# Optimization experiments

Hardware: AMD Instinct MI355X
Metric: run time of the kernel (lower is better)

The kernel has to match this reference:

```python
import jax, jax.numpy as jnp
import numpy as np

B, L, D, DI = 2, 2048, 1024, 2048  # batch, seq, d_model, d_inner = d_model*expand
EPS = 1e-5
N_ITERS = 30  # fixed-point iterations (no_grad phase); original iterates to convergence (max_iter cap)


def _shift(h):
    # shift(h, 1, dim=1): h_t <- h_{t-1}, zero at t=0
    return jnp.concatenate([jnp.zeros_like(h[:, :1]), h[:, :-1]], axis=1)


def _linrec(inputs, coeffs):
    # h_t = coeffs_t * h_{t-1} + inputs_t along seq axis (axis=1)
    def comb(l, r):
        a1, b1 = l
        a2, b2 = r
        return a2 * a1, a2 * b1 + b2
    _, h = jax.lax.associative_scan(comb, (coeffs, inputs), axis=1)
    return h


def _fp_step(x_i, b, lam, W_v, b_v, h_prev):
    # channel mixing: rank-1 selective Householder reflection of delta_x,
    # parameterized by concat([x_mixer, shift(h_prev)]) (mixer_h_dep, not symm)
    h_sh = _shift(h_prev)
    param = jnp.concatenate([x_i, h_sh], axis=-1)            # [B,L,2*DI]
    v = jax.nn.silu(param @ W_v + b_v)                        # [B,L,DI]
    v = v / (jnp.linalg.norm(v, axis=-1, keepdims=True) + EPS)
    dx = b * x_i - h_prev
    mixed = dx - 2.0 * jnp.sum(dx * v, axis=-1, keepdims=True) * v
    x_tilde = mixed + h_prev
    # sequence mixing: h_t = lam_t * h_{t-1} + (1-lam_t) * x_tilde_t
    return _linrec((1.0 - lam) * x_tilde, lam)


def setup_inputs() -> dict:
    key = jax.random.key(0)
    ks = jax.random.split(key, 8)
    def w(k, shape, fan_in):
        return (jax.random.normal(k, shape, jnp.float32) / np.sqrt(fan_in)).astype(jnp.float32)
    return {
        "x": jax.random.normal(ks[0], (B, L, D), jnp.float32),
        "W_in": w(ks[1], (D, 2 * DI), D),          # input_trans (no bias)
        "W_b": w(ks[2], (DI, DI), DI),              # b_proj (no bias)
        "W_lam": w(ks[3], (DI, DI), DI),            # lambda_proj
        "b_lam": jnp.zeros((DI,), jnp.float32),
        "W_v": w(ks[4], (2 * DI, DI), 2 * DI),      # mixer householder vector proj
        "b_v": jnp.zeros((DI,), jnp.float32),
        "W_c": w(ks[5], (2 * DI, DI), 2 * DI),      # c_proj (no bias)
        "g_norm": jnp.ones((DI,), jnp.float32),     # RMSNorm weight
        "W_out": w(ks[6], (DI, D), DI),             # output_trans (no bias)
    }


def reference(x, W_in, W_b, W_lam, b_lam, W_v, b_v, W_c, g_norm, W_out):
    xz = x @ W_in                                   # [B,L,2*DI]
    x_i, z = xz[..., :DI], xz[..., DI:]
    # no short conv: x_mixer = x_b = x_lambda = x_i
    b = jax.nn.silu(x_i @ W_b)
    lam = jax.nn.sigmoid(x_i @ W_lam + b_lam)

    step = lambda h: _fp_step(x_i, b, lam, W_v, b_v, h)
    # fixed-point iteration (no grad in original)
    h0 = jax.lax.fori_loop(0, N_ITERS, lambda i, h: step(h), jnp.zeros_like(x_i))
    # n_backwards = 1 differentiable step
    h = step(h0)

    x_c = jnp.concatenate([x_i, _shift(h)], axis=-1)
    c = jax.nn.silu(x_c @ W_c)
    y = c * h
    u = jax.nn.silu(z) * y
    u = u * jax.lax.rsqrt(jnp.mean(u * u, axis=-1, keepdims=True) + EPS) * g_norm  # RMSNorm
    return u @ W_out
```

## Files before the change

kernel.cpp:

```cpp
#include <hip/hip_runtime.h>
#include <hip/hip_bf16.h>
#include <hip/hip_fp16.h>

#define DI     2048
#define LSEQ   2048
#define NBATCH 2
#define MROWS  4096
#define EPSF   1e-5f
#define NSTEPS 31
#define NCH    64
#define CL     32

typedef float    f32x4 __attribute__((ext_vector_type(4)));
typedef float    f32x2 __attribute__((ext_vector_type(2)));
typedef _Float16 f16x8 __attribute__((ext_vector_type(8)));
typedef _Float16 f16x2 __attribute__((ext_vector_type(2)));
using f16 = _Float16;

constexpr size_t MB = 1024ull * 1024ull;
constexpr size_t OFF_APARAM = 0;
constexpr size_t OFF_WVT    = OFF_APARAM + 32 * MB;
constexpr size_t OFF_WCT    = OFF_WVT    + 16 * MB;
constexpr size_t OFF_WBT    = OFF_WCT    + 16 * MB;
constexpr size_t OFF_WLT    = OFF_WBT    +  8 * MB;
constexpr size_t OFF_WINT   = OFF_WLT    +  8 * MB;
constexpr size_t OFF_WOT    = OFF_WINT   +  8 * MB;
constexpr size_t OFF_AX     = OFF_WOT    +  4 * MB;
constexpr size_t OFF_Z      = OFF_AX     +  8 * MB;
constexpr size_t OFF_U      = OFF_Z      + 16 * MB;
constexpr size_t OFF_XI     = OFF_U      + 16 * MB;
constexpr size_t OFF_BX     = OFF_XI     + 32 * MB;
constexpr size_t OFF_LAM    = OFF_BX     + 32 * MB;
constexpr size_t OFF_H      = OFF_LAM    + 32 * MB;
constexpr size_t OFF_VRAW   = OFF_H      + 32 * MB;
constexpr size_t OFF_VX     = OFF_VRAW   + 32 * MB;
constexpr size_t OFF_INP    = OFF_VX     + 32 * MB;
constexpr size_t OFF_SSP    = OFF_INP    + 32 * MB;
constexpr size_t OFF_DRP    = OFF_SSP    + (size_t)4096*32*4;
constexpr size_t OFF_CA     = OFF_DRP    + (size_t)4096*32*4;
constexpr size_t OFF_CB     = OFF_CA     + (size_t)NBATCH*NCH*2048*4;
constexpr size_t OFF_CAR    = OFF_CB     + (size_t)NBATCH*NCH*2048*4;
constexpr size_t ARENA_SZ   = OFF_CAR    + (size_t)NBATCH*NCH*2048*4;

__device__ __align__(256) char g_buf[ARENA_SZ];

__device__ __forceinline__ void gload16(const void* g, void* l) {
  __builtin_amdgcn_global_load_lds((const __attribute__((address_space(1))) void*)g,
                                   (__attribute__((address_space(3))) void*)l, 16, 0, 0);
}
__device__ __forceinline__ float siluf(float x) { return x / (1.0f + __expf(-x)); }
__device__ __forceinline__ float sigmf(float x) { return 1.0f / (1.0f + __expf(-x)); }

template<int EPI>
__global__ __launch_bounds__(256) void gemm_f16(
    const f16* __restrict__ A, int lda,
    const f16* __restrict__ Bt, int ldb,
    int N, int K,
    float* __restrict__ outf,
    f16* __restrict__ outb,
    f16* __restrict__ outb2,
    const float* __restrict__ aux0,
    const float* __restrict__ aux1,
    const float* __restrict__ aux2,
    const f16* __restrict__ auxb,
    float* __restrict__ ssp,
    float* __restrict__ drp)
{
  __shared__ char As[2][128 * 64 * 2];
  __shared__ char Bs[2][128 * 64 * 2];

  const int tid = threadIdx.x;
  const int l   = tid & 63;
  const int w   = tid >> 6;
  const int wm  = (w >> 1) << 6;
  const int wn  = (w & 1) << 6;
  const int ntn = N >> 7;
  const int nwg = (int)gridDim.x;
  const int id  = (blockIdx.x & 7) * (nwg >> 3) + (blockIdx.x >> 3);
  const int bm  = id / ntn;
  const int bn  = id % ntn;
  const size_t m0 = (size_t)bm << 7;
  const size_t n0 = (size_t)bn << 7;

  const char* Ab = (const char*)A + m0 * (size_t)(lda * 2);
  const char* Bb = (const char*)Bt + n0 * (size_t)(ldb * 2);

  f32x4 acc[4][4];
#pragma unroll
  for (int i = 0; i < 4; ++i)
#pragma unroll
    for (int j = 0; j < 4; ++j) acc[i][j] = (f32x4){0.f, 0.f, 0.f, 0.f};

  auto stage = [&](int bf, int kte) {
#pragma unroll
    for (int rep = 0; rep < 4; ++rep) {
      const int o   = tid + (rep << 8);
      const int r   = o >> 3;
      const int cb  = (o & 7) << 4;
      const int scb = cb ^ ((r & 7) << 4);
      gload16(Ab + (size_t)r * (size_t)(lda * 2) + (size_t)kte * 2 + scb, &As[bf][o << 4]);
      gload16(Bb + (size_t)r * (size_t)(ldb * 2) + (size_t)kte * 2 + scb, &Bs[bf][o << 4]);
    }
  };

  const int nt = K >> 6;
  stage(0, 0);
  for (int t = 0; t < nt; ++t) {
    const int cur = t & 1;
    if (t + 1 < nt) {
      stage(cur ^ 1, (t + 1) << 6);
      asm volatile("s_waitcnt vmcnt(8)" ::: "memory");
    } else {
      asm volatile("s_waitcnt vmcnt(0)" ::: "memory");
    }
    __builtin_amdgcn_s_barrier();
    __builtin_amdgcn_sched_barrier(0);
    const char* Asc = As[cur];
    const char* Bsc = Bs[cur];
#pragma unroll
    for (int kk = 0; kk < 2; ++kk) {
      f16x8 af[4], bfr[4];
      const int kb = (kk << 6) + ((l >> 4) << 4);
#pragma unroll
      for (int i = 0; i < 4; ++i) {
        const int Ra = wm + (i << 4) + (l & 15);
        af[i]  = *(const f16x8*)(Asc + (Ra << 7) + (kb ^ ((Ra & 7) << 4)));
        const int Rb = wn + (i << 4) + (l & 15);
        bfr[i] = *(const f16x8*)(Bsc + (Rb << 7) + (kb ^ ((Rb & 7) << 4)));
      }
#pragma unroll
      for (int i = 0; i < 4; ++i)
#pragma unroll
        for (int j = 0; j < 4; ++j)
          acc[i][j] = __builtin_amdgcn_mfma_f32_16x16x32_f16(af[i], bfr[j], acc[i][j], 0, 0, 0);
    }
    __builtin_amdgcn_sched_barrier(0);
    __builtin_amdgcn_s_barrier();
    __builtin_amdgcn_sched_barrier(0);
  }

  if constexpr (EPI == 4) {
#pragma unroll
    for (int i = 0; i < 4; ++i) {
#pragma unroll
      for (int rg = 0; rg < 4; ++rg) {
        const size_t row = m0 + wm + (i << 4) + ((l >> 4) << 2) + rg;
        float ssl = 0.f, drl = 0.f;
#pragma unroll
        for (int j = 0; j < 4; ++j) {
          const size_t col = n0 + wn + (j << 4) + (l & 15);
          const size_t idx = (row << 11) + col;
          const float v = siluf(acc[i][j][rg] + aux2[idx]);
          outf[idx] = v;
          ssl += v * v;
          drl += (aux0[idx] - aux1[idx]) * v;
        }
#pragma unroll
        for (int m = 8; m; m >>= 1) {
          ssl += __shfl_xor(ssl, m);
          drl += __shfl_xor(drl, m);
        }
        if ((l & 15) == 0) {
          const int nb2 = (bn << 1) + (wn >> 6);
          ssp[(row << 5) + nb2] = ssl;
          drp[(row << 5) + nb2] = drl;
        }
      }
    }
  } else {
#pragma unroll
    for (int i = 0; i < 4; ++i) {
#pragma unroll
      for (int j = 0; j < 4; ++j) {
#pragma unroll
        for (int rg = 0; rg < 4; ++rg) {
          const size_t row = m0 + wm + (i << 4) + ((l >> 4) << 2) + rg;
          const size_t col = n0 + wn + (j << 4) + (l & 15);
          const float v = acc[i][j][rg];
          if constexpr (EPI == 0) {
            outf[row * (size_t)N + col] = v;
          } else if constexpr (EPI == 1) {
            if (col < DI) {
              outf[(row << 11) + col] = v;
              outb[(row << 12) + col] = (f16)v;
            } else {
              outb2[(row << 11) + (col - DI)] = (f16)v;
            }
          } else if constexpr (EPI == 2) {
            const size_t idx = (row << 11) + col;
            outf[idx] = siluf(v) * aux0[idx];
          } else if constexpr (EPI == 3) {
            outf[(row << 11) + col] = sigmf(v + aux1[col]);
          } else if constexpr (EPI == 5) {
            const size_t idx = (row << 11) + col;
            outf[idx] = siluf(v) * aux0[idx] * siluf((float)auxb[idx]);
          } else if constexpr (EPI == 6) {
            const size_t idx = (row << 11) + col;
            outf[idx] = v + aux1[col];
          }
        }
      }
    }
  }
}

__global__ __launch_bounds__(256) void transpose_f32_f16(
    const float* __restrict__ in, f16* __restrict__ out, int R, int C)
{
  __shared__ float t[32][33];
  const int bx = blockIdx.x * 32;
  const int by = blockIdx.y * 32;
  const int lx = threadIdx.x;
  const int ly = threadIdx.y;
#pragma unroll
  for (int i = 0; i < 32; i += 8)
    t[ly + i][lx] = in[(size_t)(by + ly + i) * C + bx + lx];
  __syncthreads();
#pragma unroll
  for (int i = 0; i < 32; i += 8)
    out[(size_t)(bx + ly + i) * R + by + lx] = (f16)t[lx][ly + i];
}

__global__ __launch_bounds__(256) void cast_f32_f16(
    const float* __restrict__ in, f16* __restrict__ out, int n)
{
  const int i = blockIdx.x * 256 + threadIdx.x;
  if (i < n) out[i] = (f16)in[i];
}

__global__ __launch_bounds__(256) void fill_init(
    float* __restrict__ h, f16* __restrict__ Aparam)
{
  const int idx = blockIdx.x * 256 + threadIdx.x;
  h[idx] = 0.0f;
  const int r = idx >> 11, c = idx & 2047;
  Aparam[((size_t)r << 12) + DI + c] = (f16)0.0f;
}

__global__ __launch_bounds__(256) void scan_k1(
    const float* __restrict__ vraw, const float* __restrict__ bx,
    const float* __restrict__ lam,
    const float* __restrict__ ssp, const float* __restrict__ drp,
    float* __restrict__ inp, float* __restrict__ cA, float* __restrict__ cB)
{
  const int bid = blockIdx.x;
  const int g  = bid & 3;
  const int ch = (bid >> 2) & (NCH - 1);
  const int b  = bid >> 8;
  const int tid = threadIdx.x;
  const int d = (g << 9) + (tid << 1);

  __shared__ float sc_s[CL];
  if (tid < CL) {
    const int grow = b * LSEQ + ch * CL + tid;
    float ss = 0.f, dr = 0.f;
#pragma unroll
    for (int p = 0; p < 32; ++p) {
      ss += ssp[(grow << 5) + p];
      dr += drp[(grow << 5) + p];
    }
    const float n = sqrtf(ss) + EPSF;
    sc_s[tid] = 2.0f * dr / (n * n);
  }
  __syncthreads();

  const size_t base = ((size_t)(b * LSEQ + ch * CL) << 11) + d;
  float hv0 = 0.f, hv1 = 0.f, A0 = 1.f, A1 = 1.f;
#pragma unroll 4
  for (int t = 0; t < CL; ++t) {
    const size_t ix = base + ((size_t)t << 11);
    const f32x2 la = *(const f32x2*)&lam[ix];
    const f32x2 v  = *(const f32x2*)&vraw[ix];
    const f32x2 bb = *(const f32x2*)&bx[ix];
    const float sc = sc_s[t];
    const float i0 = (1.0f - la.x) * (bb.x - sc * v.x);
    const float i1 = (1.0f - la.y) * (bb.y - sc * v.y);
    *(f32x2*)&inp[ix] = (f32x2){i0, i1};
    hv0 = la.x * hv0 + i0;
    hv1 = la.y * hv1 + i1;
    A0 *= la.x;
    A1 *= la.y;
  }
  const size_t ci = ((size_t)(b * NCH + ch) << 11) + d;
  *(f32x2*)&cA[ci] = (f32x2){A0, A1};
  *(f32x2*)&cB[ci] = (f32x2){hv0, hv1};
}

__global__ __launch_bounds__(256) void scan_carry(
    const float* __restrict__ cA, const float* __restrict__ cB,
    float* __restrict__ carry)
{
  const int idx = blockIdx.x * 256 + threadIdx.x;
  const int b = idx >> 11, d = idx & 2047;
  float cur = 0.f;
  for (int ch = 0; ch < NCH; ++ch) {
    const size_t ci = ((size_t)(b * NCH + ch) << 11) + d;
    carry[ci] = cur;
    cur = cA[ci] * cur + cB[ci];
  }
}

__global__ __launch_bounds__(256) void scan_k2(
    const float* __restrict__ inp, const float* __restrict__ lam,
    const float* __restrict__ carry,
    float* __restrict__ h, f16* __restrict__ Aparam)
{
  const int bid = blockIdx.x;
  const int g  = bid & 3;
  const int ch = (bid >> 2) & (NCH - 1);
  const int b  = bid >> 8;
  const int tid = threadIdx.x;
  const int d = (g << 9) + (tid << 1);

  const size_t ci = ((size_t)(b * NCH + ch) << 11) + d;
  const f32x2 cr = *(const f32x2*)&carry[ci];
  float hv0 = cr.x, hv1 = cr.y;

  const size_t base = ((size_t)(b * LSEQ + ch * CL) << 11) + d;
#pragma unroll 4
  for (int t = 0; t < CL; ++t) {
    const size_t ix = base + ((size_t)t << 11);
    const f32x2 la = *(const f32x2*)&lam[ix];
    const f32x2 ii = *(const f32x2*)&inp[ix];
    hv0 = la.x * hv0 + ii.x;
    hv1 = la.y * hv1 + ii.y;
    *(f32x2*)&h[ix] = (f32x2){hv0, hv1};
    const int tg = ch * CL + t;
    if (tg < LSEQ - 1)
      *(f16x2*)&Aparam[(((size_t)(b * LSEQ + tg + 1)) << 12) + DI + d] =
          (f16x2){(f16)hv0, (f16)hv1};
  }
}

__global__ __launch_bounds__(256) void rms_norm(
    const float* __restrict__ uraw, const float* __restrict__ gn,
    f16* __restrict__ u)
{
  const int row = blockIdx.x;
  const size_t base = (size_t)row << 11;
  const int tid = threadIdx.x;
  float uv[8];
  float ss = 0.f;
#pragma unroll
  for (int k = 0; k < 8; ++k) {
    const int c = tid + (k << 8);
    uv[k] = uraw[base + c];
    ss += uv[k] * uv[k];
  }
#pragma unroll
  for (int off = 32; off; off >>= 1) ss += __shfl_xor(ss, off);
  __shared__ float sred[4];
  const int l = tid & 63, w = tid >> 6;
  if (l == 0) sred[w] = ss;
  __syncthreads();
  ss = sred[0] + sred[1] + sred[2] + sred[3];
  const float scale = 1.0f / sqrtf(ss * (1.0f / DI) + EPSF);
#pragma unroll
  for (int k = 0; k < 8; ++k) {
    const int c = tid + (k << 8);
    u[base + c] = (f16)(uv[k] * scale * gn[c]);
  }
}

extern "C" void kernel_launch(void* const* d_in, const int* in_sizes, int n_in,
                              void* d_out, int out_size, void* d_ws, size_t ws_size,
                              hipStream_t stream)
{
  (void)in_sizes; (void)n_in; (void)out_size; (void)d_ws; (void)ws_size;
  const float* x      = (const float*)d_in[0];
  const float* W_in   = (const float*)d_in[1];
  const float* W_b    = (const float*)d_in[2];
  const float* W_lam  = (const float*)d_in[3];
  const float* b_lam  = (const float*)d_in[4];
  const float* W_v    = (const float*)d_in[5];
  const float* b_v    = (const float*)d_in[6];
  const float* W_c    = (const float*)d_in[7];
  const float* g_norm = (const float*)d_in[8];
  const float* W_out  = (const float*)d_in[9];
  float* out = (float*)d_out;

  char* buf = nullptr;
  hipGetSymbolAddress((void**)&buf, HIP_SYMBOL(g_buf));

  f16* Aparam = (f16*)(buf + OFF_APARAM);
  f16* Wvt    = (f16*)(buf + OFF_WVT);
  f16* Wct    = (f16*)(buf + OFF_WCT);
  f16* Wbt    = (f16*)(buf + OFF_WBT);
  f16* Wlt    = (f16*)(buf + OFF_WLT);
  f16* Wint   = (f16*)(buf + OFF_WINT);
  f16* Wot    = (f16*)(buf + OFF_WOT);
  f16* Ax     = (f16*)(buf + OFF_AX);
  f16* Zb     = (f16*)(buf + OFF_Z);
  f16* Ub     = (f16*)(buf + OFF_U);
  float* xi   = (float*)(buf + OFF_XI);
  float* bx   = (float*)(buf + OFF_BX);
  float* lam  = (float*)(buf + OFF_LAM);
  float* h    = (float*)(buf + OFF_H);
  float* vraw = (float*)(buf + OFF_VRAW);
  float* vx   = (float*)(buf + OFF_VX);
  float* inp  = (float*)(buf + OFF_INP);
  float* ssp  = (float*)(buf + OFF_SSP);
  float* drp  = (float*)(buf + OFF_DRP);
  float* cA   = (float*)(buf + OFF_CA);
  float* cB   = (float*)(buf + OFF_CB);
  float* car  = (float*)(buf + OFF_CAR);

  const dim3 b256(256);
  const dim3 tb(32, 8);

  fill_init<<<dim3(MROWS * DI / 256), b256, 0, stream>>>(h, Aparam);

  transpose_f32_f16<<<dim3(4096 / 32, 1024 / 32), tb, 0, stream>>>(W_in,  Wint, 1024, 4096);
  transpose_f32_f16<<<dim3(2048 / 32, 2048 / 32), tb, 0, stream>>>(W_b,   Wbt,  2048, 2048);
  transpose_f32_f16<<<dim3(2048 / 32, 2048 / 32), tb, 0, stream>>>(W_lam, Wlt,  2048, 2048);
  transpose_f32_f16<<<dim3(2048 / 32, 4096 / 32), tb, 0, stream>>>(W_v,   Wvt,  4096, 2048);
  transpose_f32_f16<<<dim3(2048 / 32, 4096 / 32), tb, 0, stream>>>(W_c,   Wct,  4096, 2048);
  transpose_f32_f16<<<dim3(1024 / 32, 2048 / 32), tb, 0, stream>>>(W_out, Wot,  2048, 1024);
  cast_f32_f16<<<dim3(MROWS * 1024 / 256), b256, 0, stream>>>(x, Ax, MROWS * 1024);

  gemm_f16<1><<<dim3(32 * 32), b256, 0, stream>>>(Ax, 1024, Wint, 1024, 4096, 1024,
      xi, Aparam, Zb, nullptr, nullptr, nullptr, nullptr, nullptr, nullptr);
  gemm_f16<2><<<dim3(32 * 16), b256, 0, stream>>>(Aparam, 4096, Wbt, 2048, 2048, 2048,
      bx, nullptr, nullptr, xi, nullptr, nullptr, nullptr, nullptr, nullptr);
  gemm_f16<3><<<dim3(32 * 16), b256, 0, stream>>>(Aparam, 4096, Wlt, 2048, 2048, 2048,
      lam, nullptr, nullptr, nullptr, b_lam, nullptr, nullptr, nullptr, nullptr);
  gemm_f16<6><<<dim3(32 * 16), b256, 0, stream>>>(Aparam, 4096, Wvt, 4096, 2048, 2048,
      vx, nullptr, nullptr, nullptr, b_v, nullptr, nullptr, nullptr, nullptr);

  for (int s = 0; s < NSTEPS; ++s) {
    gemm_f16<4><<<dim3(32 * 16), b256, 0, stream>>>(Aparam + DI, 4096, Wvt + DI, 4096, 2048, 2048,
        vraw, nullptr, nullptr, bx, h, vx, nullptr, ssp, drp);
    scan_k1<<<dim3(NBATCH * NCH * 4), b256, 0, stream>>>(vraw, bx, lam, ssp, drp, inp, cA, cB);
    scan_carry<<<dim3(16), b256, 0, stream>>>(cA, cB, car);
    scan_k2<<<dim3(NBATCH * NCH * 4), b256, 0, stream>>>(inp, lam, car, h, Aparam);
  }

  gemm_f16<5><<<dim3(32 * 16), b256, 0, stream>>>(Aparam, 4096, Wct, 4096, 2048, 4096,
      vraw, nullptr, nullptr, h, nullptr, nullptr, Zb, nullptr, nullptr);
  rms_norm<<<dim3(MROWS), b256, 0, stream>>>(vraw, g_norm, Ub);
  gemm_f16<0><<<dim3(32 * 8), b256, 0, stream>>>(Ub, 2048, Wot, 2048, 1024, 2048,
      out, nullptr, nullptr, nullptr, nullptr, nullptr, nullptr, nullptr, nullptr);
}
```

Before: 3.701 ms.

## Use 8-wave GEMM blocks and fold carry scan into second scan pass

```diff
diff --git a/kernel.cpp b/kernel.cpp
--- a/kernel.cpp
+++ b/kernel.cpp
@@ -36,11 +36,10 @@
 constexpr size_t OFF_VX     = OFF_VRAW   + 32 * MB;
 constexpr size_t OFF_INP    = OFF_VX     + 32 * MB;
 constexpr size_t OFF_SSP    = OFF_INP    + 32 * MB;
-constexpr size_t OFF_DRP    = OFF_SSP    + (size_t)4096*32*4;
-constexpr size_t OFF_CA     = OFF_DRP    + (size_t)4096*32*4;
+constexpr size_t OFF_DRP    = OFF_SSP    + (size_t)4096*64*4;
+constexpr size_t OFF_CA     = OFF_DRP    + (size_t)4096*64*4;
 constexpr size_t OFF_CB     = OFF_CA     + (size_t)NBATCH*NCH*2048*4;
-constexpr size_t OFF_CAR    = OFF_CB     + (size_t)NBATCH*NCH*2048*4;
-constexpr size_t ARENA_SZ   = OFF_CAR    + (size_t)NBATCH*NCH*2048*4;
+constexpr size_t ARENA_SZ   = OFF_CB     + (size_t)NBATCH*NCH*2048*4;
 
 __device__ __align__(256) char g_buf[ARENA_SZ];
 
@@ -52,7 +51,7 @@
 __device__ __forceinline__ float sigmf(float x) { return 1.0f / (1.0f + __expf(-x)); }
 
 template<int EPI>
-__global__ __launch_bounds__(256) void gemm_f16(
+__global__ __launch_bounds__(512) void gemm_f16(
     const f16* __restrict__ A, int lda,
     const f16* __restrict__ Bt, int ldb,
     int N, int K,
@@ -72,8 +71,8 @@
   const int tid = threadIdx.x;
   const int l   = tid & 63;
   const int w   = tid >> 6;
-  const int wm  = (w >> 1) << 6;
-  const int wn  = (w & 1) << 6;
+  const int wm  = (w >> 2) << 6;
+  const int wn  = (w & 3) << 5;
   const int ntn = N >> 7;
   const int nwg = (int)gridDim.x;
   const int id  = (blockIdx.x & 7) * (nwg >> 3) + (blockIdx.x >> 3);
@@ -85,16 +84,16 @@
   const char* Ab = (const char*)A + m0 * (size_t)(lda * 2);
   const char* Bb = (const char*)Bt + n0 * (size_t)(ldb * 2);
 
-  f32x4 acc[4][4];
+  f32x4 acc[4][2];
 #pragma unroll
   for (int i = 0; i < 4; ++i)
 #pragma unroll
-    for (int j = 0; j < 4; ++j) acc[i][j] = (f32x4){0.f, 0.f, 0.f, 0.f};
+    for (int j = 0; j < 2; ++j) acc[i][j] = (f32x4){0.f, 0.f, 0.f, 0.f};
 
   auto stage = [&](int bf, int kte) {
 #pragma unroll
-    for (int rep = 0; rep < 4; ++rep) {
-      const int o   = tid + (rep << 8);
+    for (int rep = 0; rep < 2; ++rep) {
+      const int o   = tid + (rep << 9);
       const int r   = o >> 3;
       const int cb  = (o & 7) << 4;
       const int scb = cb ^ ((r & 7) << 4);
@@ -109,7 +108,7 @@
     const int cur = t & 1;
     if (t + 1 < nt) {
       stage(cur ^ 1, (t + 1) << 6);
-      asm volatile("s_waitcnt vmcnt(8)" ::: "memory");
+      asm volatile("s_waitcnt vmcnt(4)" ::: "memory");
     } else {
       asm volatile("s_waitcnt vmcnt(0)" ::: "memory");
     }
@@ -119,19 +118,22 @@
     const char* Bsc = Bs[cur];
 #pragma unroll
     for (int kk = 0; kk < 2; ++kk) {
-      f16x8 af[4], bfr[4];
+      f16x8 af[4], bfr[2];
       const int kb = (kk << 6) + ((l >> 4) << 4);
 #pragma unroll
       for (int i = 0; i < 4; ++i) {
         const int Ra = wm + (i << 4) + (l & 15);
-        af[i]  = *(const f16x8*)(Asc + (Ra << 7) + (kb ^ ((Ra & 7) << 4)));
-        const int Rb = wn + (i << 4) + (l & 15);
-        bfr[i] = *(const f16x8*)(Bsc + (Rb << 7) + (kb ^ ((Rb & 7) << 4)));
+        af[i] = *(const f16x8*)(Asc + (Ra << 7) + (kb ^ ((Ra & 7) << 4)));
       }
 #pragma unroll
+      for (int j = 0; j < 2; ++j) {
+        const int Rb = wn + (j << 4) + (l & 15);
+        bfr[j] = *(const f16x8*)(Bsc + (Rb << 7) + (kb ^ ((Rb & 7) << 4)));
+      }
+#pragma unroll
       for (int i = 0; i < 4; ++i)
 #pragma unroll
-        for (int j = 0; j < 4; ++j)
+        for (int j = 0; j < 2; ++j)
           acc[i][j] = __builtin_amdgcn_mfma_f32_16x16x32_f16(af[i], bfr[j], acc[i][j], 0, 0, 0);
     }
     __builtin_amdgcn_sched_barrier(0);
@@ -147,7 +149,7 @@
         const size_t row = m0 + wm + (i << 4) + ((l >> 4) << 2) + rg;
         float ssl = 0.f, drl = 0.f;
 #pragma unroll
-        for (int j = 0; j < 4; ++j) {
+        for (int j = 0; j < 2; ++j) {
           const size_t col = n0 + wn + (j << 4) + (l & 15);
           const size_t idx = (row << 11) + col;
           const float v = siluf(acc[i][j][rg] + aux2[idx]);
@@ -161,9 +163,9 @@
           drl += __shfl_xor(drl, m);
         }
         if ((l & 15) == 0) {
-          const int nb2 = (bn << 1) + (wn >> 6);
-          ssp[(row << 5) + nb2] = ssl;
-          drp[(row << 5) + nb2] = drl;
+          const int nb = (int)((n0 + wn) >> 5);
+          ssp[(row << 6) + nb] = ssl;
+          drp[(row << 6) + nb] = drl;
         }
       }
     }
@@ -171,7 +173,7 @@
 #pragma unroll
     for (int i = 0; i < 4; ++i) {
 #pragma unroll
-      for (int j = 0; j < 4; ++j) {
+      for (int j = 0; j < 2; ++j) {
 #pragma unroll
         for (int rg = 0; rg < 4; ++rg) {
           const size_t row = m0 + wm + (i << 4) + ((l >> 4) << 2) + rg;
@@ -255,9 +257,9 @@
     const int grow = b * LSEQ + ch * CL + tid;
     float ss = 0.f, dr = 0.f;
 #pragma unroll
-    for (int p = 0; p < 32; ++p) {
-      ss += ssp[(grow << 5) + p];
-      dr += drp[(grow << 5) + p];
+    for (int p = 0; p < 64; ++p) {
+      ss += ssp[(grow << 6) + p];
+      dr += drp[(grow << 6) + p];
     }
     const float n = sqrtf(ss) + EPSF;
     sc_s[tid] = 2.0f * dr / (n * n);
@@ -286,23 +288,9 @@
   *(f32x2*)&cB[ci] = (f32x2){hv0, hv1};
 }
 
-__global__ __launch_bounds__(256) void scan_carry(
-    const float* __restrict__ cA, const float* __restrict__ cB,
-    float* __restrict__ carry)
-{
-  const int idx = blockIdx.x * 256 + threadIdx.x;
-  const int b = idx >> 11, d = idx & 2047;
-  float cur = 0.f;
-  for (int ch = 0; ch < NCH; ++ch) {
-    const size_t ci = ((size_t)(b * NCH + ch) << 11) + d;
-    carry[ci] = cur;
-    cur = cA[ci] * cur + cB[ci];
-  }
-}
-
 __global__ __launch_bounds__(256) void scan_k2(
     const float* __restrict__ inp, const float* __restrict__ lam,
-    const float* __restrict__ carry,
+    const float* __restrict__ cA, const float* __restrict__ cB,
     float* __restrict__ h, f16* __restrict__ Aparam)
 {
   const int bid = blockIdx.x;
@@ -312,9 +300,14 @@
   const int tid = threadIdx.x;
   const int d = (g << 9) + (tid << 1);
 
-  const size_t ci = ((size_t)(b * NCH + ch) << 11) + d;
-  const f32x2 cr = *(const f32x2*)&carry[ci];
-  float hv0 = cr.x, hv1 = cr.y;
+  float hv0 = 0.f, hv1 = 0.f;
+  for (int cc = 0; cc < ch; ++cc) {
+    const size_t ci = ((size_t)(b * NCH + cc) << 11) + d;
+    const f32x2 a  = *(const f32x2*)&cA[ci];
+    const f32x2 bb = *(const f32x2*)&cB[ci];
+    hv0 = a.x * hv0 + bb.x;
+    hv1 = a.y * hv1 + bb.y;
+  }
 
   const size_t base = ((size_t)(b * LSEQ + ch * CL) << 11) + d;
 #pragma unroll 4
@@ -403,9 +396,9 @@
   float* drp  = (float*)(buf + OFF_DRP);
   float* cA   = (float*)(buf + OFF_CA);
   float* cB   = (float*)(buf + OFF_CB);
-  float* car  = (float*)(buf + OFF_CAR);
 
   const dim3 b256(256);
+  const dim3 b512(512);
   const dim3 tb(32, 8);
 
   fill_init<<<dim3(MROWS * DI / 256), b256, 0, stream>>>(h, Aparam);
@@ -418,26 +411,25 @@
   transpose_f32_f16<<<dim3(1024 / 32, 2048 / 32), tb, 0, stream>>>(W_out, Wot,  2048, 1024);
   cast_f32_f16<<<dim3(MROWS * 1024 / 256), b256, 0, stream>>>(x, Ax, MROWS * 1024);
 
-  gemm_f16<1><<<dim3(32 * 32), b256, 0, stream>>>(Ax, 1024, Wint, 1024, 4096, 1024,
+  gemm_f16<1><<<dim3(32 * 32), b512, 0, stream>>>(Ax, 1024, Wint, 1024, 4096, 1024,
       xi, Aparam, Zb, nullptr, nullptr, nullptr, nullptr, nullptr, nullptr);
-  gemm_f16<2><<<dim3(32 * 16), b256, 0, stream>>>(Aparam, 4096, Wbt, 2048, 2048, 2048,
+  gemm_f16<2><<<dim3(32 * 16), b512, 0, stream>>>(Aparam, 4096, Wbt, 2048, 2048, 2048,
       bx, nullptr, nullptr, xi, nullptr, nullptr, nullptr, nullptr, nullptr);
-  gemm_f16<3><<<dim3(32 * 16), b256, 0, stream>>>(Aparam, 4096, Wlt, 2048, 2048, 2048,
+  gemm_f16<3><<<dim3(32 * 16), b512, 0, stream>>>(Aparam, 4096, Wlt, 2048, 2048, 2048,
       lam, nullptr, nullptr, nullptr, b_lam, nullptr, nullptr, nullptr, nullptr);
-  gemm_f16<6><<<dim3(32 * 16), b256, 0, stream>>>(Aparam, 4096, Wvt, 4096, 2048, 2048,
+  gemm_f16<6><<<dim3(32 * 16), b512, 0, stream>>>(Aparam, 4096, Wvt, 4096, 2048, 2048,
       vx, nullptr, nullptr, nullptr, b_v, nullptr, nullptr, nullptr, nullptr);
 
   for (int s = 0; s < NSTEPS; ++s) {
-    gemm_f16<4><<<dim3(32 * 16), b256, 0, stream>>>(Aparam + DI, 4096, Wvt + DI, 4096, 2048, 2048,
+    gemm_f16<4><<<dim3(32 * 16), b512, 0, stream>>>(Aparam + DI, 4096, Wvt + DI, 4096, 2048, 2048,
         vraw, nullptr, nullptr, bx, h, vx, nullptr, ssp, drp);
     scan_k1<<<dim3(NBATCH * NCH * 4), b256, 0, stream>>>(vraw, bx, lam, ssp, drp, inp, cA, cB);
-    scan_carry<<<dim3(16), b256, 0, stream>>>(cA, cB, car);
-    scan_k2<<<dim3(NBATCH * NCH * 4), b256, 0, stream>>>(inp, lam, car, h, Aparam);
-  }
-
-  gemm_f16<5><<<dim3(32 * 16), b256, 0, stream>>>(Aparam, 4096, Wct, 4096, 2048, 4096,
+    scan_k2<<<dim3(NBATCH * NCH * 4), b256, 0, stream>>>(inp, lam, cA, cB, h, Aparam);
+  }
+
+  gemm_f16<5><<<dim3(32 * 16), b512, 0, stream>>>(Aparam, 4096, Wct, 4096, 2048, 4096,
       vraw, nullptr, nullptr, h, nullptr, nullptr, Zb, nullptr, nullptr);
   rms_norm<<<dim3(MROWS), b256, 0, stream>>>(vraw, g_norm, Ub);
-  gemm_f16<0><<<dim3(32 * 8), b256, 0, stream>>>(Ub, 2048, Wot, 2048, 1024, 2048,
+  gemm_f16<0><<<dim3(32 * 8), b512, 0, stream>>>(Ub, 2048, Wot, 2048, 1024, 2048,
       out, nullptr, nullptr, nullptr, nullptr, nullptr, nullptr, nullptr, nullptr);
 }
```

After: 3.761 ms. Within noise of the previous version (+1.6%).
